# Kernel tuning notes

Hardware: AMD Instinct MI355X
Metric: run time of the kernel (lower is better)

The kernel has to match this reference:

```python
import math
import jax, jax.numpy as jnp
import numpy as np

NUM_HEADS = 8
ATTN_STD = [1.0] * 8                 # per-head gaussian std (broadcast from len-1 config)
ATTN_OFFSET = [-3, -2, -1, 0, 0, 1, 2, 3]  # per-head positional offset
ATTN_THRESHOLD = -1.0                # <=0 means no thresholding
WORD_COUNT_RATIO = 1.0


def gaussian_attn(qlen, vlen, dtype=jnp.float32):
    """Hard-coded positional attention weights, [H, qlen, vlen].
    Equivalent to get_attn_cache + offset-shifted fancy indexing:
    w[h,q,v] = N(v - offset_h - q*ratio; 0, std_h) pdf value."""
    std = jnp.asarray(ATTN_STD, jnp.float32)[:, None, None]
    ofs = jnp.asarray(ATTN_OFFSET, jnp.float32)[:, None, None]
    q = jnp.arange(qlen, dtype=jnp.float32)[None, :, None] * WORD_COUNT_RATIO
    v = jnp.arange(vlen, dtype=jnp.float32)[None, None, :]
    diff = (v - ofs) - q
    logits = jnp.exp(-0.5 * (diff / std) ** 2) / (std * math.sqrt(2.0 * math.pi))
    if ATTN_THRESHOLD > 0:
        logits = jnp.where(logits < ATTN_THRESHOLD, 0.0, logits)
    return logits.astype(dtype)


def setup_inputs() -> dict:
    key = jax.random.key(0)
    k0, k1, k2, k3 = jax.random.split(key, 4)
    B, L, E = 8, 1024, 1024
    values = jax.random.normal(k0, (B, L, E), jnp.float32)
    queries = jax.random.normal(k1, (B, L, E), jnp.float32)
    key_mask = jnp.zeros((B, L), dtype=bool)
    # xavier-ish scale for linear weights
    input_weights = jax.random.normal(k2, (E, E), jnp.float32) * (1.0 / math.sqrt(E))
    output_weight = jax.random.normal(k3, (E, E), jnp.float32) * (1.0 / math.sqrt(E))
    return {"values": values, "queries": queries, "key_mask": key_mask,
            "input_weights": input_weights, "output_weight": output_weight}


def reference(values, queries, key_mask, input_weights, output_weight):
    B, Lv, E = values.shape
    Lq = queries.shape[1]
    H = NUM_HEADS
    d = E // H
    # value projection (F.linear: x @ W.T), split into heads: [B, H, Lv, d]
    v = (values @ input_weights.T).reshape(B, Lv, H, d).transpose(0, 2, 1, 3)
    # masked_fill_ on padded key positions
    v = jnp.where(key_mask[:, None, :, None], 0.0, v)
    attn = gaussian_attn(Lq, Lv)                     # [H, Lq, Lv] shared over batch
    attended = jnp.einsum('hqv,bhvd->bhqd', attn, v)  # [B, H, Lq, d]
    out = attended.transpose(0, 2, 1, 3).reshape(B, Lq, E)  # mha_reshape
    return out @ output_weight.T                     # output_projection (no bias)
```

## Files before the change

### kernel.cpp

```cpp
#include <hip/hip_runtime.h>
#include <hip/hip_bf16.h>
#include <cstddef>


#define BATCH 8
#define SEQL  1024
#define EMB   1024
#define VROWS 1056

typedef unsigned short u16;
typedef __attribute__((ext_vector_type(8))) short s16x8;
typedef __attribute__((ext_vector_type(4))) float f32x4;
typedef __attribute__((ext_vector_type(8))) unsigned short u16x8;
typedef __attribute__((ext_vector_type(4))) unsigned short u16x4;

#define GLOAD_LDS16(g, l)                                                     \
    __builtin_amdgcn_global_load_lds(                                         \
        (const __attribute__((address_space(1))) void*)(g),                   \
        (__attribute__((address_space(3))) void*)(l), 16, 0, 0)

__device__ __forceinline__ u16 f2bf(float f) {
    unsigned u = __builtin_bit_cast(unsigned, f);
    u += 0x7FFF + ((u >> 16) & 1);
    return (u16)(u >> 16);
}

__constant__ int c_ofs[8] = { -3, -2, -1, 0, 0, 1, 2, 3 };

__global__ __launch_bounds__(256) void smooth_lds(
    const float* __restrict__ values, const unsigned char* __restrict__ mask,
    const float* __restrict__ wi, const float* __restrict__ wo,
    u16* __restrict__ VG, u16* __restrict__ wib, u16* __restrict__ wob)
{
    constexpr float W[9] = {
        1.3383022576488537e-04f, 4.431848411938008e-03f, 5.399096651318806e-02f,
        2.4197072451914337e-01f, 3.989422804014327e-01f, 2.4197072451914337e-01f,
        5.399096651318806e-02f,  4.431848411938008e-03f, 1.3383022576488537e-04f
    };
    __shared__ float sx[40 * 256];
    __shared__ float smf[40];

    const int blk = blockIdx.x;
    const int NSM = BATCH * 33 * 4;
    const int tid = threadIdx.x;
    if (blk < NSM) {
        const int b  = blk & 7;
        const int t  = blk >> 3;
        const int g  = t >> 2;
        const int cg = t & 3;
        const int r0 = g * 32;
        const int v0 = r0 - 8;
        const int c0 = cg * 256;
        const float* vbase = values + (size_t)b * SEQL * EMB + c0;
        const unsigned char* mrow = mask + b * SEQL;

        #pragma unroll
        for (int c = 0; c < 10; ++c) {
            const int n    = c * 256 + tid;
            const int row  = n >> 6;
            const int col4 = (n & 63) * 4;
            const int v    = v0 + row;
            const int vc   = v < 0 ? 0 : (v > SEQL - 1 ? SEQL - 1 : v);
            GLOAD_LDS16(vbase + (size_t)vc * EMB + col4,
                        sx + c * 1024 + (tid >> 6) * 256);
        }
        if (tid < 40) {
            const int v  = v0 + tid;
            const int vc = v < 0 ? 0 : (v > SEQL - 1 ? SEQL - 1 : v);
            smf[tid] = ((unsigned)v < (unsigned)SEQL && !mrow[vc]) ? 1.f : 0.f;
        }
        asm volatile("s_waitcnt vmcnt(0)" ::: "memory");
        __syncthreads();

        const int rg = tid >> 6;
        const int cc = tid & 63;
        const int rl0 = rg * 8;
        f32x4 acc[8] = {};
        #pragma unroll
        for (int i = 0; i < 16; ++i) {
            const f32x4 xr = *(const f32x4*)&sx[(rl0 + i) * 256 + cc * 4];
            const float f = smf[rl0 + i];
            const float x0 = xr[0] * f, x1 = xr[1] * f, x2 = xr[2] * f, x3 = xr[3] * f;
            #pragma unroll
            for (int k = 0; k < 8; ++k) {
                const int j = i - k;
                if (j < 0 || j > 8) continue;
                const float w = W[j];
                acc[k][0] = fmaf(w, x0, acc[k][0]);
                acc[k][1] = fmaf(w, x1, acc[k][1]);
                acc[k][2] = fmaf(w, x2, acc[k][2]);
                acc[k][3] = fmaf(w, x3, acc[k][3]);
            }
        }
        u16* og = VG + (size_t)(b * VROWS + r0 + rl0) * EMB + c0 + cc * 4;
        #pragma unroll
        for (int k = 0; k < 8; ++k) {
            u16x4 o;
            o[0] = f2bf(acc[k][0]); o[1] = f2bf(acc[k][1]);
            o[2] = f2bf(acc[k][2]); o[3] = f2bf(acc[k][3]);
            *(u16x4*)(og + (size_t)k * EMB) = o;
        }
    } else {
        const int k = (blk - NSM) * 256 + tid;
        const float* src = (k < 131072) ? wi : wo;
        u16* dst = (k < 131072) ? wib : wob;
        const size_t off = (size_t)(k & 131071) * 8;
        const float4 a = *(const float4*)(src + off);
        const float4 b4 = *(const float4*)(src + off + 4);
        u16x8 o;
        o[0] = f2bf(a.x);  o[1] = f2bf(a.y);  o[2] = f2bf(a.z);  o[3] = f2bf(a.w);
        o[4] = f2bf(b4.x); o[5] = f2bf(b4.y); o[6] = f2bf(b4.z); o[7] = f2bf(b4.w);
        *(u16x8*)(dst + off) = o;
    }
}

constexpr int BM = 256, BN = 128, BK = 64;
constexpr int A_EL = BM * BK;
constexpr int B_EL = BN * BK;
constexpr int BUF_EL = A_EL + B_EL;

template <bool OUT_BF16, bool SHIFTED>
__global__ __launch_bounds__(512, 2) void gemm_nt_pipe(
    const u16* __restrict__ A, const u16* __restrict__ B,
    void* __restrict__ Cout, int M, int N, int K)
{
    __shared__ u16 lds[3 * BUF_EL];

    const int tid  = threadIdx.x;
    const int lane = tid & 63;
    const int wave = tid >> 6;

    const int nwg = gridDim.x;
    const int bid = blockIdx.x;
    const int swz = (bid & 7) * (nwg >> 3) + (bid >> 3);
    const int ntn = N >> 7;
    const int row0 = (swz / ntn) * BM;
    const int col0 = (swz % ntn) * BN;

    int arow0;
    if (SHIFTED) {
        const int b  = row0 >> 10;
        const int q0 = row0 & (SEQL - 1);
        arow0 = b * VROWS + q0 + 4 + c_ofs[col0 >> 7];
    } else {
        arow0 = row0;
    }
    const u16* Ab = A + (size_t)arow0 * K;
    const u16* Bb = B + (size_t)col0 * K;

    const int wm = wave >> 1;
    const int wn = wave & 1;
    const int fr = lane & 15;
    const int fg = lane >> 4;

    const int srow   = tid >> 3;
    const int schunk = tid & 7;

    f32x4 acc[4][4] = {};
    s16x8 af[4][2], bf0[2][2], bf1[2][2];

    auto stageA3 = [&](int bsel, int kt) {
        u16* Abuf = lds + bsel * BUF_EL;
        const int k0 = kt << 6;
        #pragma unroll
        for (int c = 0; c < 3; ++c) {
            const int row = c * 64 + srow;
            const int sc  = (schunk ^ (row & 7)) << 3;
            GLOAD_LDS16(Ab + (size_t)row * K + k0 + sc, Abuf + c * 4096 + wave * 512);
        }
    };
    auto stageRest = [&](int bsel, int kt) {
        u16* Abuf = lds + bsel * BUF_EL;
        u16* Bbuf = Abuf + A_EL;
        const int k0 = kt << 6;
        {
            const int row = 192 + srow;
            const int sc  = (schunk ^ (row & 7)) << 3;
            GLOAD_LDS16(Ab + (size_t)row * K + k0 + sc, Abuf + 3 * 4096 + wave * 512);
        }
        #pragma unroll
        for (int c = 0; c < 2; ++c) {
            const int row = c * 64 + srow;
            const int sc  = (schunk ^ (row & 7)) << 3;
            GLOAD_LDS16(Bb + (size_t)row * K + k0 + sc, Bbuf + c * 4096 + wave * 512);
        }
    };

    auto phase0 = [&](int tile, bool doStage) {
        const u16* Abuf = lds + (tile % 3) * BUF_EL;
        const u16* Bbuf = Abuf + A_EL;
        #pragma unroll
        for (int m = 0; m < 4; ++m)
            #pragma unroll
            for (int kk = 0; kk < 2; ++kk) {
                const int row = wm * 64 + m * 16 + fr;
                const int ch  = ((kk << 2) + fg) ^ (row & 7);
                af[m][kk] = *(const s16x8*)(Abuf + row * 64 + ch * 8);
            }
        #pragma unroll
        for (int n = 0; n < 2; ++n)
            #pragma unroll
            for (int kk = 0; kk < 2; ++kk) {
                const int row = wn * 64 + n * 16 + fr;
                const int ch  = ((kk << 2) + fg) ^ (row & 7);
                bf0[n][kk] = *(const s16x8*)(Bbuf + row * 64 + ch * 8);
            }
        if (doStage) stageA3((tile + 2) % 3, tile + 2);
        __builtin_amdgcn_s_barrier();
        asm volatile("s_waitcnt lgkmcnt(0)" ::: "memory");
        __builtin_amdgcn_sched_barrier(0);
        __builtin_amdgcn_s_setprio(1);
        #pragma unroll
        for (int m = 0; m < 4; ++m)
            #pragma unroll
            for (int n = 0; n < 2; ++n)
                #pragma unroll
                for (int kk = 0; kk < 2; ++kk)
                    acc[m][n] = __builtin_amdgcn_mfma_f32_16x16x32_bf16(
                        af[m][kk], bf0[n][kk], acc[m][n], 0, 0, 0);
        __builtin_amdgcn_s_setprio(0);
        __builtin_amdgcn_s_barrier();
    };

    auto phase1 = [&](int tile, int mode ) {
        const u16* Abuf = lds + (tile % 3) * BUF_EL;
        const u16* Bbuf = Abuf + A_EL;
        #pragma unroll
        for (int n = 0; n < 2; ++n)
            #pragma unroll
            for (int kk = 0; kk < 2; ++kk) {
                const int row = wn * 64 + (2 + n) * 16 + fr;
                const int ch  = ((kk << 2) + fg) ^ (row & 7);
                bf1[n][kk] = *(const s16x8*)(Bbuf + row * 64 + ch * 8);
            }
        if (mode == 0) {
            stageRest((tile + 2) % 3, tile + 2);
            asm volatile("s_waitcnt vmcnt(6)" ::: "memory");
        } else if (mode == 1) {
            asm volatile("s_waitcnt vmcnt(0)" ::: "memory");
        }
        __builtin_amdgcn_s_barrier();
        asm volatile("s_waitcnt lgkmcnt(0)" ::: "memory");
        __builtin_amdgcn_sched_barrier(0);
        __builtin_amdgcn_s_setprio(1);
        #pragma unroll
        for (int m = 0; m < 4; ++m)
            #pragma unroll
            for (int n = 0; n < 2; ++n)
                #pragma unroll
                for (int kk = 0; kk < 2; ++kk)
                    acc[m][2 + n] = __builtin_amdgcn_mfma_f32_16x16x32_bf16(
                        af[m][kk], bf1[n][kk], acc[m][2 + n], 0, 0, 0);
        __builtin_amdgcn_s_setprio(0);
        __builtin_amdgcn_s_barrier();
    };

    const int NT = K >> 6;

    stageA3(0, 0); stageRest(0, 0);
    stageA3(1, 1); stageRest(1, 1);
    asm volatile("s_waitcnt vmcnt(6)" ::: "memory");
    __builtin_amdgcn_s_barrier();

    for (int t = 0; t < NT - 2; ++t) { phase0(t, true); phase1(t, 0); }
    phase0(NT - 2, false); phase1(NT - 2, 1);
    phase0(NT - 1, false); phase1(NT - 1, 2);

    const int crow0 = row0 + wm * 64 + fg * 4;
    const int ccol0 = col0 + wn * 64 + fr;
    if (OUT_BF16) {
        u16* C = (u16*)Cout;
        #pragma unroll
        for (int m = 0; m < 4; ++m)
            #pragma unroll
            for (int n = 0; n < 4; ++n)
                #pragma unroll
                for (int j = 0; j < 4; ++j)
                    C[(size_t)(crow0 + m * 16 + j) * N + ccol0 + n * 16] =
                        f2bf(acc[m][n][j]);
    } else {
        float* C = (float*)Cout;
        #pragma unroll
        for (int m = 0; m < 4; ++m)
            #pragma unroll
            for (int n = 0; n < 4; ++n)
                #pragma unroll
                for (int j = 0; j < 4; ++j)
                    C[(size_t)(crow0 + m * 16 + j) * N + ccol0 + n * 16] =
                        acc[m][n][j];
    }
}

extern "C" void kernel_launch(void* const* d_in, const int* in_sizes, int n_in,
                              void* d_out, int out_size, void* d_ws, size_t ws_size,
                              hipStream_t stream) {
    const float* values = (const float*)d_in[0];
    const unsigned char* mask = (const unsigned char*)d_in[2];
    const float* Win  = (const float*)d_in[3];
    const float* Wout = (const float*)d_in[4];
    float* out = (float*)d_out;

    const int M = BATCH * SEQL;
    const int N = EMB;
    const int K = EMB;

    u16* VG    = (u16*)d_ws;
    u16* Attb  = VG + (size_t)BATCH * VROWS * EMB;
    u16* Winb  = Attb + (size_t)M * EMB;
    u16* Woutb = Winb + (size_t)EMB * EMB;

    smooth_lds<<<1056 + 1024, 256, 0, stream>>>(
        values, mask, Win, Wout, VG, Winb, Woutb);

    dim3 ggrid((M / BM) * (N / BN));
    gemm_nt_pipe<true,  true ><<<ggrid, 512, 0, stream>>>(VG,   Winb,  Attb, M, N, K);
    gemm_nt_pipe<false, false><<<ggrid, 512, 0, stream>>>(Attb, Woutb, out,  M, N, K);
}
```

Baseline: 61.03 us.

## Switch GEMM to 32x32x16 MFMA with single-phase tile loop

Replaces the 16x16x32 bf16 MFMA tiling (4x4 fragments per wave, split into two phases) with 32x32x16 MFMA on 2x2 fragments per wave. Each K-tile is handled in one phase that reads all A/B fragments, issues the whole next-tile stage at once, and needs one barrier instead of two or more. This aims to cut LDS fragment reads per FLOP and barrier overhead. In exchange, the staging loads and MFMA work no longer interleave across two phases, which can reduce overlap, and the larger fragment set raises register pressure.

```diff
diff --git a/kernel.cpp b/kernel.cpp
--- a/kernel.cpp
+++ b/kernel.cpp
@@ -11,6 +11,7 @@
 typedef unsigned short u16;
 typedef __attribute__((ext_vector_type(8))) short s16x8;
 typedef __attribute__((ext_vector_type(4))) float f32x4;
+typedef __attribute__((ext_vector_type(16))) float f32x16;
 typedef __attribute__((ext_vector_type(8))) unsigned short u16x8;
 typedef __attribute__((ext_vector_type(4))) unsigned short u16x4;
 
@@ -148,35 +149,25 @@
     const u16* Ab = A + (size_t)arow0 * K;
     const u16* Bb = B + (size_t)col0 * K;
 
-    const int wm = wave >> 1;
-    const int wn = wave & 1;
-    const int fr = lane & 15;
-    const int fg = lane >> 4;
+    const int wm  = wave >> 1;
+    const int wn  = wave & 1;
+    const int l31 = lane & 31;
+    const int lhi = lane >> 5;
 
     const int srow   = tid >> 3;
     const int schunk = tid & 7;
 
-    f32x4 acc[4][4] = {};
-    s16x8 af[4][2], bf0[2][2], bf1[2][2];
-
-    auto stageA3 = [&](int bsel, int kt) {
+    f32x16 acc[2][2] = {};
+
+    auto stageAll = [&](int bsel, int kt) {
         u16* Abuf = lds + bsel * BUF_EL;
+        u16* Bbuf = Abuf + A_EL;
         const int k0 = kt << 6;
         #pragma unroll
-        for (int c = 0; c < 3; ++c) {
+        for (int c = 0; c < 4; ++c) {
             const int row = c * 64 + srow;
             const int sc  = (schunk ^ (row & 7)) << 3;
             GLOAD_LDS16(Ab + (size_t)row * K + k0 + sc, Abuf + c * 4096 + wave * 512);
-        }
-    };
-    auto stageRest = [&](int bsel, int kt) {
-        u16* Abuf = lds + bsel * BUF_EL;
-        u16* Bbuf = Abuf + A_EL;
-        const int k0 = kt << 6;
-        {
-            const int row = 192 + srow;
-            const int sc  = (schunk ^ (row & 7)) << 3;
-            GLOAD_LDS16(Ab + (size_t)row * K + k0 + sc, Abuf + 3 * 4096 + wave * 512);
         }
         #pragma unroll
         for (int c = 0; c < 2; ++c) {
@@ -186,108 +177,78 @@
         }
     };
 
-    auto phase0 = [&](int tile, bool doStage) {
+    auto doTile = [&](int tile, int mode ) {
         const u16* Abuf = lds + (tile % 3) * BUF_EL;
         const u16* Bbuf = Abuf + A_EL;
-        #pragma unroll
-        for (int m = 0; m < 4; ++m)
-            #pragma unroll
-            for (int kk = 0; kk < 2; ++kk) {
-                const int row = wm * 64 + m * 16 + fr;
-                const int ch  = ((kk << 2) + fg) ^ (row & 7);
-                af[m][kk] = *(const s16x8*)(Abuf + row * 64 + ch * 8);
+        s16x8 a[2][4], b[2][4];
+        #pragma unroll
+        for (int ks = 0; ks < 4; ++ks) {
+            const int cb = ks * 2 + lhi;
+            #pragma unroll
+            for (int m = 0; m < 2; ++m) {
+                const int row = wm * 64 + m * 32 + l31;
+                a[m][ks] = *(const s16x8*)(Abuf + row * 64 + ((cb ^ (row & 7)) << 3));
             }
-        #pragma unroll
-        for (int n = 0; n < 2; ++n)
-            #pragma unroll
-            for (int kk = 0; kk < 2; ++kk) {
-                const int row = wn * 64 + n * 16 + fr;
-                const int ch  = ((kk << 2) + fg) ^ (row & 7);
-                bf0[n][kk] = *(const s16x8*)(Bbuf + row * 64 + ch * 8);
+            #pragma unroll
+            for (int n = 0; n < 2; ++n) {
+                const int row = wn * 64 + n * 32 + l31;
+                b[n][ks] = *(const s16x8*)(Bbuf + row * 64 + ((cb ^ (row & 7)) << 3));
             }
-        if (doStage) stageA3((tile + 2) % 3, tile + 2);
-        __builtin_amdgcn_s_barrier();
+        }
+        if (mode == 0) {
+            stageAll((tile + 2) % 3, tile + 2);
+            asm volatile("s_waitcnt vmcnt(6)" ::: "memory");
+        } else if (mode == 1) {
+            asm volatile("s_waitcnt vmcnt(0)" ::: "memory");
+        }
         asm volatile("s_waitcnt lgkmcnt(0)" ::: "memory");
         __builtin_amdgcn_sched_barrier(0);
         __builtin_amdgcn_s_setprio(1);
         #pragma unroll
-        for (int m = 0; m < 4; ++m)
-            #pragma unroll
-            for (int n = 0; n < 2; ++n)
+        for (int ks = 0; ks < 4; ++ks)
+            #pragma unroll
+            for (int m = 0; m < 2; ++m)
                 #pragma unroll
-                for (int kk = 0; kk < 2; ++kk)
-                    acc[m][n] = __builtin_amdgcn_mfma_f32_16x16x32_bf16(
-                        af[m][kk], bf0[n][kk], acc[m][n], 0, 0, 0);
+                for (int n = 0; n < 2; ++n)
+                    acc[m][n] = __builtin_amdgcn_mfma_f32_32x32x16_bf16(
+                        a[m][ks], b[n][ks], acc[m][n], 0, 0, 0);
         __builtin_amdgcn_s_setprio(0);
         __builtin_amdgcn_s_barrier();
     };
 
-    auto phase1 = [&](int tile, int mode ) {
-        const u16* Abuf = lds + (tile % 3) * BUF_EL;
-        const u16* Bbuf = Abuf + A_EL;
-        #pragma unroll
-        for (int n = 0; n < 2; ++n)
-            #pragma unroll
-            for (int kk = 0; kk < 2; ++kk) {
-                const int row = wn * 64 + (2 + n) * 16 + fr;
-                const int ch  = ((kk << 2) + fg) ^ (row & 7);
-                bf1[n][kk] = *(const s16x8*)(Bbuf + row * 64 + ch * 8);
-            }
-        if (mode == 0) {
-            stageRest((tile + 2) % 3, tile + 2);
-            asm volatile("s_waitcnt vmcnt(6)" ::: "memory");
-        } else if (mode == 1) {
-            asm volatile("s_waitcnt vmcnt(0)" ::: "memory");
-        }
-        __builtin_amdgcn_s_barrier();
-        asm volatile("s_waitcnt lgkmcnt(0)" ::: "memory");
-        __builtin_amdgcn_sched_barrier(0);
-        __builtin_amdgcn_s_setprio(1);
-        #pragma unroll
-        for (int m = 0; m < 4; ++m)
+    const int NT = K >> 6;
+
+    stageAll(0, 0);
+    stageAll(1, 1);
+    asm volatile("s_waitcnt vmcnt(6)" ::: "memory");
+    __builtin_amdgcn_s_barrier();
+
+    for (int t = 0; t < NT - 2; ++t) doTile(t, 0);
+    doTile(NT - 2, 1);
+    doTile(NT - 1, 2);
+
+    const int crow_b = row0 + wm * 64 + 4 * lhi;
+    const int ccol_b = col0 + wn * 64 + l31;
+    if (OUT_BF16) {
+        u16* C = (u16*)Cout;
+        #pragma unroll
+        for (int m = 0; m < 2; ++m)
             #pragma unroll
             for (int n = 0; n < 2; ++n)
                 #pragma unroll
-                for (int kk = 0; kk < 2; ++kk)
-                    acc[m][2 + n] = __builtin_amdgcn_mfma_f32_16x16x32_bf16(
-                        af[m][kk], bf1[n][kk], acc[m][2 + n], 0, 0, 0);
-        __builtin_amdgcn_s_setprio(0);
-        __builtin_amdgcn_s_barrier();
-    };
-
-    const int NT = K >> 6;
-
-    stageA3(0, 0); stageRest(0, 0);
-    stageA3(1, 1); stageRest(1, 1);
-    asm volatile("s_waitcnt vmcnt(6)" ::: "memory");
-    __builtin_amdgcn_s_barrier();
-
-    for (int t = 0; t < NT - 2; ++t) { phase0(t, true); phase1(t, 0); }
-    phase0(NT - 2, false); phase1(NT - 2, 1);
-    phase0(NT - 1, false); phase1(NT - 1, 2);
-
-    const int crow0 = row0 + wm * 64 + fg * 4;
-    const int ccol0 = col0 + wn * 64 + fr;
-    if (OUT_BF16) {
-        u16* C = (u16*)Cout;
-        #pragma unroll
-        for (int m = 0; m < 4; ++m)
-            #pragma unroll
-            for (int n = 0; n < 4; ++n)
-                #pragma unroll
-                for (int j = 0; j < 4; ++j)
-                    C[(size_t)(crow0 + m * 16 + j) * N + ccol0 + n * 16] =
-                        f2bf(acc[m][n][j]);
+                for (int r = 0; r < 16; ++r)
+                    C[(size_t)(crow_b + m * 32 + (r & 3) + 8 * (r >> 2)) * N
+                      + ccol_b + n * 32] = f2bf(acc[m][n][r]);
     } else {
         float* C = (float*)Cout;
         #pragma unroll
-        for (int m = 0; m < 4; ++m)
-            #pragma unroll
-            for (int n = 0; n < 4; ++n)
+        for (int m = 0; m < 2; ++m)
+            #pragma unroll
+            for (int n = 0; n < 2; ++n)
                 #pragma unroll
-                for (int j = 0; j < 4; ++j)
-                    C[(size_t)(crow0 + m * 16 + j) * N + ccol0 + n * 16] =
-                        acc[m][n][j];
+                for (int r = 0; r < 16; ++r)
+                    C[(size_t)(crow_b + m * 32 + (r & 3) + 8 * (r >> 2)) * N
+                      + ccol_b + n * 32] = acc[m][n][r];
     }
 }
 
```

Result: slower. 63.08 us (+3.4%).

## Shrink GEMM tiles to 128x128x32 with 256-thread blocks and single-phase pipeline

Applied to the files above, without the earlier changes.

Reduces the GEMM block tile from 256x128x64 with 512 threads to 128x128x32 with 256 threads. The two-phase split of each K-tile is replaced by one stage-and-compute step per 32-wide K slice, with a 4-chunk XOR swizzle matching the narrower LDS rows. This doubles the grid so more workgroups fill the CUs and cuts LDS use per block. In exchange each tile reuses loaded data less and pays more barriers per unit of K.

```diff
diff --git a/kernel.cpp b/kernel.cpp
--- a/kernel.cpp
+++ b/kernel.cpp
@@ -114,13 +114,13 @@
     }
 }
 
-constexpr int BM = 256, BN = 128, BK = 64;
+constexpr int BM = 128, BN = 128, BK = 32;
 constexpr int A_EL = BM * BK;
 constexpr int B_EL = BN * BK;
 constexpr int BUF_EL = A_EL + B_EL;
 
 template <bool OUT_BF16, bool SHIFTED>
-__global__ __launch_bounds__(512, 2) void gemm_nt_pipe(
+__global__ __launch_bounds__(256, 2) void gemm_nt_pipe(
     const u16* __restrict__ A, const u16* __restrict__ B,
     void* __restrict__ Cout, int M, int N, int K)
 {
@@ -153,59 +153,54 @@
     const int fr = lane & 15;
     const int fg = lane >> 4;
 
-    const int srow   = tid >> 3;
-    const int schunk = tid & 7;
-
     f32x4 acc[4][4] = {};
-    s16x8 af[4][2], bf0[2][2], bf1[2][2];
-
-    auto stageA3 = [&](int bsel, int kt) {
-        u16* Abuf = lds + bsel * BUF_EL;
-        const int k0 = kt << 6;
-        #pragma unroll
-        for (int c = 0; c < 3; ++c) {
-            const int row = c * 64 + srow;
-            const int sc  = (schunk ^ (row & 7)) << 3;
-            GLOAD_LDS16(Ab + (size_t)row * K + k0 + sc, Abuf + c * 4096 + wave * 512);
-        }
-    };
-    auto stageRest = [&](int bsel, int kt) {
+
+    auto stage = [&](int bsel, int ht) {
         u16* Abuf = lds + bsel * BUF_EL;
         u16* Bbuf = Abuf + A_EL;
-        const int k0 = kt << 6;
-        {
-            const int row = 192 + srow;
-            const int sc  = (schunk ^ (row & 7)) << 3;
-            GLOAD_LDS16(Ab + (size_t)row * K + k0 + sc, Abuf + 3 * 4096 + wave * 512);
-        }
-        #pragma unroll
-        for (int c = 0; c < 2; ++c) {
-            const int row = c * 64 + srow;
-            const int sc  = (schunk ^ (row & 7)) << 3;
-            GLOAD_LDS16(Bb + (size_t)row * K + k0 + sc, Bbuf + c * 4096 + wave * 512);
+        const int k0 = ht << 5;
+        #pragma unroll
+        for (int i = 0; i < 2; ++i) {
+            const int n   = i * 256 + tid;
+            const int row = n >> 2;
+            const int c   = n & 3;
+            const int sc  = (c ^ ((row >> 1) & 3)) << 3;
+            GLOAD_LDS16(Ab + (size_t)row * K + k0 + sc,
+                        Abuf + i * 2048 + wave * 512);
+        }
+        #pragma unroll
+        for (int i = 0; i < 2; ++i) {
+            const int n   = i * 256 + tid;
+            const int row = n >> 2;
+            const int c   = n & 3;
+            const int sc  = (c ^ ((row >> 1) & 3)) << 3;
+            GLOAD_LDS16(Bb + (size_t)row * K + k0 + sc,
+                        Bbuf + i * 2048 + wave * 512);
         }
     };
 
-    auto phase0 = [&](int tile, bool doStage) {
-        const u16* Abuf = lds + (tile % 3) * BUF_EL;
+    auto doHalf = [&](int ht, int mode ) {
+        const u16* Abuf = lds + (ht % 3) * BUF_EL;
         const u16* Bbuf = Abuf + A_EL;
-        #pragma unroll
-        for (int m = 0; m < 4; ++m)
-            #pragma unroll
-            for (int kk = 0; kk < 2; ++kk) {
-                const int row = wm * 64 + m * 16 + fr;
-                const int ch  = ((kk << 2) + fg) ^ (row & 7);
-                af[m][kk] = *(const s16x8*)(Abuf + row * 64 + ch * 8);
-            }
-        #pragma unroll
-        for (int n = 0; n < 2; ++n)
-            #pragma unroll
-            for (int kk = 0; kk < 2; ++kk) {
-                const int row = wn * 64 + n * 16 + fr;
-                const int ch  = ((kk << 2) + fg) ^ (row & 7);
-                bf0[n][kk] = *(const s16x8*)(Bbuf + row * 64 + ch * 8);
-            }
-        if (doStage) stageA3((tile + 2) % 3, tile + 2);
+        s16x8 af[4], bf[4];
+        #pragma unroll
+        for (int m = 0; m < 4; ++m) {
+            const int row = wm * 64 + m * 16 + fr;
+            const int cb  = fg ^ ((row >> 1) & 3);
+            af[m] = *(const s16x8*)(Abuf + row * 32 + cb * 8);
+        }
+        #pragma unroll
+        for (int n = 0; n < 4; ++n) {
+            const int row = wn * 64 + n * 16 + fr;
+            const int cb  = fg ^ ((row >> 1) & 3);
+            bf[n] = *(const s16x8*)(Bbuf + row * 32 + cb * 8);
+        }
+        if (mode == 0) {
+            stage((ht + 2) % 3, ht + 2);
+            asm volatile("s_waitcnt vmcnt(4)" ::: "memory");
+        } else if (mode == 1) {
+            asm volatile("s_waitcnt vmcnt(0)" ::: "memory");
+        }
         __builtin_amdgcn_s_barrier();
         asm volatile("s_waitcnt lgkmcnt(0)" ::: "memory");
         __builtin_amdgcn_sched_barrier(0);
@@ -213,58 +208,23 @@
         #pragma unroll
         for (int m = 0; m < 4; ++m)
             #pragma unroll
-            for (int n = 0; n < 2; ++n)
-                #pragma unroll
-                for (int kk = 0; kk < 2; ++kk)
-                    acc[m][n] = __builtin_amdgcn_mfma_f32_16x16x32_bf16(
-                        af[m][kk], bf0[n][kk], acc[m][n], 0, 0, 0);
+            for (int n = 0; n < 4; ++n)
+                acc[m][n] = __builtin_amdgcn_mfma_f32_16x16x32_bf16(
+                    af[m], bf[n], acc[m][n], 0, 0, 0);
         __builtin_amdgcn_s_setprio(0);
         __builtin_amdgcn_s_barrier();
     };
 
-    auto phase1 = [&](int tile, int mode ) {
-        const u16* Abuf = lds + (tile % 3) * BUF_EL;
-        const u16* Bbuf = Abuf + A_EL;
-        #pragma unroll
-        for (int n = 0; n < 2; ++n)
-            #pragma unroll
-            for (int kk = 0; kk < 2; ++kk) {
-                const int row = wn * 64 + (2 + n) * 16 + fr;
-                const int ch  = ((kk << 2) + fg) ^ (row & 7);
-                bf1[n][kk] = *(const s16x8*)(Bbuf + row * 64 + ch * 8);
-            }
-        if (mode == 0) {
-            stageRest((tile + 2) % 3, tile + 2);
-            asm volatile("s_waitcnt vmcnt(6)" ::: "memory");
-        } else if (mode == 1) {
-            asm volatile("s_waitcnt vmcnt(0)" ::: "memory");
-        }
-        __builtin_amdgcn_s_barrier();
-        asm volatile("s_waitcnt lgkmcnt(0)" ::: "memory");
-        __builtin_amdgcn_sched_barrier(0);
-        __builtin_amdgcn_s_setprio(1);
-        #pragma unroll
-        for (int m = 0; m < 4; ++m)
-            #pragma unroll
-            for (int n = 0; n < 2; ++n)
-                #pragma unroll
-                for (int kk = 0; kk < 2; ++kk)
-                    acc[m][2 + n] = __builtin_amdgcn_mfma_f32_16x16x32_bf16(
-                        af[m][kk], bf1[n][kk], acc[m][2 + n], 0, 0, 0);
-        __builtin_amdgcn_s_setprio(0);
-        __builtin_amdgcn_s_barrier();
-    };
-
-    const int NT = K >> 6;
-
-    stageA3(0, 0); stageRest(0, 0);
-    stageA3(1, 1); stageRest(1, 1);
-    asm volatile("s_waitcnt vmcnt(6)" ::: "memory");
+    const int NH = K >> 5;
+
+    stage(0, 0);
+    stage(1, 1);
+    asm volatile("s_waitcnt vmcnt(4)" ::: "memory");
     __builtin_amdgcn_s_barrier();
 
-    for (int t = 0; t < NT - 2; ++t) { phase0(t, true); phase1(t, 0); }
-    phase0(NT - 2, false); phase1(NT - 2, 1);
-    phase0(NT - 1, false); phase1(NT - 1, 2);
+    for (int h = 0; h < NH - 2; ++h) doHalf(h, 0);
+    doHalf(NH - 2, 1);
+    doHalf(NH - 1, 2);
 
     const int crow0 = row0 + wm * 64 + fg * 4;
     const int ccol0 = col0 + wn * 64 + fr;
@@ -313,6 +273,6 @@
         values, mask, Win, Wout, VG, Winb, Woutb);
 
     dim3 ggrid((M / BM) * (N / BN));
-    gemm_nt_pipe<true,  true ><<<ggrid, 512, 0, stream>>>(VG,   Winb,  Attb, M, N, K);
-    gemm_nt_pipe<false, false><<<ggrid, 512, 0, stream>>>(Attb, Woutb, out,  M, N, K);
-}
+    gemm_nt_pipe<true,  true ><<<ggrid, 256, 0, stream>>>(VG,   Winb,  Attb, M, N, K);
+    gemm_nt_pipe<false, false><<<ggrid, 256, 0, stream>>>(Attb, Woutb, out,  M, N, K);
+}
```

Measured after the change: 63.06 us. +3.3%, slower.
